# Kernel optimization log

Hardware: AMD Instinct MI355X
Metric: run time of the kernel (lower is better)

## Reference

```python
import jax, jax.numpy as jnp
import numpy as np

B, S, D_IN, D_CODE, K = 8, 4096, 1024, 64, 4096


def setup_inputs() -> dict:
    key = jax.random.key(0)
    k1, k2, k3, k4 = jax.random.split(key, 4)
    return {
        "input": jax.random.normal(k1, (B, S, D_IN), dtype=jnp.float32),
        "W_send": jax.random.normal(k2, (D_IN, D_CODE), dtype=jnp.float32) * (1.0 / np.sqrt(D_IN)),
        "b_send": jnp.zeros((D_CODE,), dtype=jnp.float32),
        "emb": jax.random.normal(k3, (K, D_CODE), dtype=jnp.float32),
        "W_recv": jax.random.normal(k4, (D_CODE, D_IN), dtype=jnp.float32) * (1.0 / np.sqrt(D_CODE)),
        "b_recv": jnp.zeros((D_IN,), dtype=jnp.float32),
    }


def reference(input, W_send, b_send, emb, W_recv, b_recv):
    # encoder: z = send(input) -> [B, S, D_CODE]
    z = jnp.einsum('bsi,ic->bsc', input, W_send) + b_send

    # VQEmbedding.lookup: argmin_k ||e_k||^2 - 2 <z, e_k>  (no-grad path)
    sqr = jnp.sum(emb * emb, axis=1)                      # [K]
    cov = jnp.einsum('bsc,kc->bsk', z, emb)               # [B, S, K]
    indices = jnp.argmin(sqr - 2.0 * cov, axis=-1)        # [B, S] int

    # fetch embeddings (gather)
    vectors = emb[indices]                                # [B, S, D_CODE]

    # straight-through estimator: values = z + sg(vectors - z)
    values = z + jax.lax.stop_gradient(vectors - z)

    # decoder: x = recv(values) -> [B, S, D_IN]
    x = jnp.einsum('bsc,ci->bsi', values, W_recv) + b_recv

    # VQEmbedding.loss (reduction='sum')
    embedding_loss = jnp.sum((vectors - jax.lax.stop_gradient(z)) ** 2)
    commitment_loss = jnp.sum((z - jax.lax.stop_gradient(vectors)) ** 2)

    # empirical code entropy in bits
    num_codes = emb.shape[0]
    counts = jnp.bincount(indices.ravel(), length=num_codes)
    p = counts.astype(jnp.float32) / jnp.float32(indices.size)
    ent = -jnp.sum(jnp.where(p > 0, p * jnp.log(jnp.where(p > 0, p, 1.0)), 0.0)) / jnp.log(2.0)

    return x, indices, embedding_loss, commitment_loss, ent
```

## Files before the change

### kernel.cpp

```cpp
#include <hip/hip_runtime.h>

#define DIN 1024
#define DC 64
#define KC 4096

typedef _Float16 f16x8 __attribute__((ext_vector_type(8)));
typedef _Float16 f16x4 __attribute__((ext_vector_type(4)));
typedef float f32x4 __attribute__((ext_vector_type(4)));

__device__ __forceinline__ void gll16(const void* g, void* l) {
    __builtin_amdgcn_global_load_lds(
        (const __attribute__((address_space(1))) unsigned int*)g,
        (__attribute__((address_space(3))) unsigned int*)l, 16, 0, 0);
}

__global__ __launch_bounds__(256) void k_prep(const float* __restrict__ emb,
                                              const float* __restrict__ Ws,
                                              const float* __restrict__ Wr,
                                              _Float16* __restrict__ Ee,
                                              float* __restrict__ sqr,
                                              _Float16* __restrict__ Wh,
                                              _Float16* __restrict__ WrT,
                                              int* __restrict__ counts) {
    int b = blockIdx.x;
    int tid = threadIdx.x;
    if (b < 1024) {
        int code = b * 4 + (tid >> 6);
        int lane = tid & 63;
        float v = emb[(size_t)code * DC + lane];
        Ee[(size_t)code * 64 + lane] = (_Float16)v;
        float s = v * v;
        #pragma unroll
        for (int m = 1; m < 64; m <<= 1) s += __shfl_xor(s, m);
        if (lane == 0) sqr[code] = s;
        if (tid < 4) counts[b * 4 + tid] = 0;
        return;
    }
    if (b < 1040) {
        int k0 = (b - 1024) * 64;
        #pragma unroll
        for (int it = 0; it < 16; ++it) {
            int q = it * 256 + tid;
            int c = q >> 6, kl = q & 63;
            float v = Ws[(size_t)(k0 + kl) * 64 + c];
            Wh[(size_t)c * 1024 + k0 + kl] = (_Float16)v;
        }
        return;
    }
    int b2 = b - 1040;
    #pragma unroll
    for (int it = 0; it < 16; ++it) {
        int k = it * 4 + (tid >> 6);
        int rr = b2 * 64 + (tid & 63);
        WrT[(size_t)rr * 64 + k] = (_Float16)Wr[(size_t)k * 1024 + rr];
    }
}

__global__ __launch_bounds__(256) void k_main(const float* __restrict__ in,
                                              const _Float16* __restrict__ Wh,
                                              const float* __restrict__ bs,
                                              const _Float16* __restrict__ Ee,
                                              const float* __restrict__ sqr,
                                              int* __restrict__ idx,
                                              float* __restrict__ out_idx,
                                              int* __restrict__ counts,
                                              float* __restrict__ lpart) {
    __shared__ char smem[32768];
    const int tid = threadIdx.x;
    const int row0 = blockIdx.x * 64;
    const int wid = tid >> 6, lane = tid & 63;
    const int c15 = lane & 15, g = lane >> 4;
    const int g16 = g * 16;
    const int wm = wid >> 1, wn = wid & 1;

    f32x4 acc[2][2];
    const f32x4 zz4 = {0.f, 0.f, 0.f, 0.f};
    #pragma unroll
    for (int mf = 0; mf < 2; ++mf)
        #pragma unroll
        for (int nf = 0; nf < 2; ++nf) acc[mf][nf] = zz4;

    int abyte[2], aswz[2], bbyte[2], bswz[2];
    #pragma unroll
    for (int mf = 0; mf < 2; ++mf) {
        int r = wm * 32 + mf * 16 + c15;
        abyte[mf] = r * 128; aswz[mf] = (r & 7) << 4;
    }
    #pragma unroll
    for (int nf = 0; nf < 2; ++nf) {
        int c = wn * 32 + nf * 16 + c15;
        bbyte[nf] = c * 128; bswz[nf] = (c & 7) << 4;
    }

    auto stageB = [&](int buf, int s) {
        char* dst = smem + buf * 16384 + 8192;
        #pragma unroll
        for (int r = 0; r < 2; ++r) {
            int p = r * 4096 + wid * 1024 + lane * 16;
            int row = p >> 7, off = p & 127;
            int soff = off ^ ((row & 7) << 4);
            gll16((const char*)Wh + (size_t)row * 2048 + s * 128 + soff,
                  dst + p);
        }
    };
    auto loadA = [&](int s, float4* a) {
        #pragma unroll
        for (int it = 0; it < 4; ++it) {
            int q = it * 256 + tid;
            int r = q >> 4, c4 = q & 15;
            a[it] = *(const float4*)&in[(size_t)(row0 + r) * DIN + s * 64 + c4 * 4];
        }
    };
    auto writeA = [&](int buf, const float4* a) {
        char* Ah = smem + buf * 16384;
        #pragma unroll
        for (int it = 0; it < 4; ++it) {
            int q = it * 256 + tid;
            int r = q >> 4, c4 = q & 15;
            float v[4] = {a[it].x, a[it].y, a[it].z, a[it].w};
            f16x4 h;
            #pragma unroll
            for (int j = 0; j < 4; ++j) h[j] = (_Float16)v[j];
            int o = r * 128 + ((c4 * 8) ^ ((r & 7) << 4));
            *(f16x4*)(Ah + o) = h;
        }
    };
    auto compute = [&](int buf) {
        const char* Ah = smem + buf * 16384;
        const char* Bh = Ah + 8192;
        #pragma unroll
        for (int ks = 0; ks < 2; ++ks) {
            int koff = ks * 64 + g16;
            f16x8 bh[2];
            #pragma unroll
            for (int nf = 0; nf < 2; ++nf)
                bh[nf] = *(const f16x8*)(Bh + bbyte[nf] + (koff ^ bswz[nf]));
            #pragma unroll
            for (int mf = 0; mf < 2; ++mf) {
                f16x8 ah = *(const f16x8*)(Ah + abyte[mf] + (koff ^ aswz[mf]));
                #pragma unroll
                for (int nf = 0; nf < 2; ++nf)
                    acc[mf][nf] = __builtin_amdgcn_mfma_f32_16x16x32_f16(
                        ah, bh[nf], acc[mf][nf], 0, 0, 0);
            }
        }
    };

    {
        float4 a0[4];
        loadA(0, a0);
        stageB(0, 0);
        writeA(0, a0);
    }
    __syncthreads();
    for (int s = 0; s < 16; ++s) {
        int c = s & 1;
        float4 an[4];
        if (s < 15) {
            loadA(s + 1, an);
            stageB(c ^ 1, s + 1);
        }
        compute(c);
        if (s < 15) writeA(c ^ 1, an);
        __syncthreads();
    }

    char* Zt = smem + 16384;
    #pragma unroll
    for (int nf = 0; nf < 2; ++nf) {
        int k = wn * 32 + nf * 16 + c15;
        float bias = bs[k];
        #pragma unroll
        for (int mf = 0; mf < 2; ++mf)
            #pragma unroll
            for (int r2 = 0; r2 < 4; ++r2) {
                int row = wm * 32 + mf * 16 + g * 4 + r2;
                _Float16 zh = (_Float16)(acc[mf][nf][r2] + bias);
                *(_Float16*)(Zt + row * 128 + ((k * 2) ^ ((row & 7) << 4))) = zh;
            }
    }
    __syncthreads();

    const int wm2 = wm, wn2 = wn;
    f16x8 zfh[2][2];
    #pragma unroll
    for (int nf = 0; nf < 2; ++nf) {
        int zr = wn2 * 32 + nf * 16 + c15;
        int sw = (zr & 7) << 4;
        #pragma unroll
        for (int j = 0; j < 2; ++j)
            zfh[j][nf] = *(const f16x8*)(Zt + zr * 128 + ((j * 64 + g16) ^ sw));
    }

    int rbase[2], rx[2];
    #pragma unroll
    for (int mf = 0; mf < 2; ++mf) {
        int r = wm2 * 32 + mf * 16 + c15;
        rbase[mf] = r * 128;
        rx[mf] = (r & 7) << 4;
    }

    auto stageE = [&](int ch, int buf) {
        char* dst = smem + buf * 8192;
        const char* src = (const char*)Ee + (size_t)ch * 8192;
        #pragma unroll
        for (int t = 0; t < 2; ++t) {
            int p = t * 4096 + tid * 16;
            int r = p >> 7, off = p & 127;
            gll16(src + r * 128 + (off ^ ((r & 7) << 4)), dst + p);
        }
    };

    float bv[2];
    int   bi[2];
    #pragma unroll
    for (int nf = 0; nf < 2; ++nf) { bv[nf] = 3.402823466e38f; bi[nf] = 0; }

    stageE(0, 0);
    __syncthreads();

    for (int ch = 0; ch < 64; ++ch) {
        const int buf = ch & 1;
        f32x4 sqv[2];
        #pragma unroll
        for (int mf = 0; mf < 2; ++mf)
            sqv[mf] = *(const f32x4*)(sqr + ch * 64 + wm2 * 32 + mf * 16 + g * 4);

        if (ch < 63) stageE(ch + 1, buf ^ 1);

        const char* base = smem + buf * 8192;
        f32x4 sacc[2][2];
        #pragma unroll
        for (int j = 0; j < 2; ++j) {
            const int kbyte = j * 64 + g16;
            f16x8 af[2];
            #pragma unroll
            for (int mf = 0; mf < 2; ++mf)
                af[mf] = *(const f16x8*)(base + rbase[mf] + (kbyte ^ rx[mf]));
            #pragma unroll
            for (int mf = 0; mf < 2; ++mf)
                #pragma unroll
                for (int nf = 0; nf < 2; ++nf)
                    sacc[mf][nf] = __builtin_amdgcn_mfma_f32_16x16x32_f16(
                        af[mf], zfh[j][nf],
                        j == 0 ? zz4 : sacc[mf][nf], 0, 0, 0);
        }

        #pragma unroll
        for (int nf = 0; nf < 2; ++nf) {
            #pragma unroll
            for (int mf = 0; mf < 2; ++mf) {
                f32x4 v = sqv[mf] - sacc[mf][nf] * 2.0f;
                #pragma unroll
                for (int r2 = 0; r2 < 4; ++r2) {
                    if (v[r2] < bv[nf]) {
                        bv[nf] = v[r2];
                        bi[nf] = ch * 64 + wm2 * 32 + mf * 16 + g * 4 + r2;
                    }
                }
            }
        }
        __syncthreads();
    }

    float* redv = (float*)(smem + 24576);
    int*   redi = (int*)(smem + 25088);
    float* zsqa = (float*)(smem + 25600);

    #pragma unroll
    for (int nf = 0; nf < 2; ++nf) {
        float v_ = bv[nf]; int i_ = bi[nf];
        #pragma unroll
        for (int m = 16; m <= 32; m <<= 1) {
            float ov = __shfl_xor(v_, m);
            int oi = __shfl_xor(i_, m);
            if (ov < v_ || (ov == v_ && oi < i_)) { v_ = ov; i_ = oi; }
        }
        if (g == 0) {
            int rl = wn2 * 32 + nf * 16 + c15;
            redv[wm2 * 64 + rl] = v_;
            redi[wm2 * 64 + rl] = i_;
        }
    }
    if (wm2 == 0) {
        #pragma unroll
        for (int nf = 0; nf < 2; ++nf) {
            float s = 0.f;
            #pragma unroll
            for (int j = 0; j < 2; ++j)
                #pragma unroll
                for (int e = 0; e < 8; ++e) {
                    float zv = (float)zfh[j][nf][e];
                    s += zv * zv;
                }
            s += __shfl_xor(s, 16);
            s += __shfl_xor(s, 32);
            if (g == 0) zsqa[wn2 * 32 + nf * 16 + c15] = s;
        }
    }
    __syncthreads();
    if (tid < 64) {
        float v0 = redv[tid]; int i0 = redi[tid];
        float v1 = redv[64 + tid]; int i1 = redi[64 + tid];
        if (v1 < v0 || (v1 == v0 && i1 < i0)) { v0 = v1; i0 = i1; }
        int grow = row0 + tid;
        idx[grow] = i0;
        out_idx[grow] = (float)i0;
        atomicAdd(&counts[i0], 1);
        float lossv = v0 + zsqa[tid];
        #pragma unroll
        for (int m = 1; m < 64; m <<= 1) lossv += __shfl_xor(lossv, m);
        if (tid == 0) lpart[blockIdx.x] = lossv;
    }
}

__global__ __launch_bounds__(256) void k_recv(const _Float16* __restrict__ Ee,
                                              const _Float16* __restrict__ WrT,
                                              const float* __restrict__ br,
                                              const int* __restrict__ idx,
                                              const int* __restrict__ counts,
                                              const float* __restrict__ lpart,
                                              float* __restrict__ x,
                                              float* __restrict__ out_sc) {
    __shared__ char smem[24832];
    int tid = threadIdx.x;

    if (blockIdx.x == 512) {
        float* red = (float*)smem;
        red[tid] = lpart[tid] + lpart[256 + tid];
        __syncthreads();
        for (int s = 128; s > 0; s >>= 1) {
            if (tid < s) red[tid] += red[tid + s];
            __syncthreads();
        }
        float loss = red[0];
        __syncthreads();
        float ep = 0.f;
        for (int k = tid; k < KC; k += 256) {
            int c = counts[k];
            if (c > 0) {
                float p = (float)c / 32768.0f;
                ep += p * logf(p);
            }
        }
        red[tid] = ep; __syncthreads();
        for (int s = 128; s > 0; s >>= 1) {
            if (tid < s) red[tid] += red[tid + s];
            __syncthreads();
        }
        if (tid == 0) {
            out_sc[0] = loss;
            out_sc[1] = loss;
            out_sc[2] = -red[0] * 1.4426950408889634f;
        }
        return;
    }

    const int row0 = blockIdx.x * 64;
    const int wid = tid >> 6, lane = tid & 63;
    const int c15 = lane & 15, g = lane >> 4;
    const int g16 = g * 16;
    int* sidx = (int*)(smem + 24576);

    if (tid < 64) sidx[tid] = idx[row0 + tid];
    __syncthreads();

    #pragma unroll
    for (int t = 0; t < 2; ++t) {
        int p = t * 4096 + tid * 16;
        int r = p >> 7, off = p & 127;
        gll16((const char*)Ee + (size_t)sidx[r] * 128 + (off ^ ((r & 7) << 4)),
              smem + p);
    }

    auto stageW = [&](int cc, int buf) {
        char* dst = smem + 8192 + buf * 8192;
        #pragma unroll
        for (int t = 0; t < 2; ++t) {
            int p = t * 4096 + tid * 16;
            int r = p >> 7, off = p & 127;
            gll16((const char*)WrT + (size_t)(cc * 64 + r) * 128
                      + (off ^ ((r & 7) << 4)),
                  dst + p);
        }
    };
    stageW(0, 0);
    __syncthreads();

    int abase[4], ax[4];
    #pragma unroll
    for (int mf = 0; mf < 4; ++mf) {
        int r = mf * 16 + c15;
        abase[mf] = r * 128;
        ax[mf] = (r & 7) << 4;
    }
    const int brow = wid * 16 + c15;
    const int bbase = 8192 + brow * 128;
    const int bx = (brow & 7) << 4;

    const f32x4 zz4 = {0.f, 0.f, 0.f, 0.f};
    for (int cc = 0; cc < 16; ++cc) {
        const int buf = cc & 1;
        if (cc < 15) stageW(cc + 1, buf ^ 1);

        const int col = cc * 64 + wid * 16 + c15;
        float bias = br[col];

        f32x4 acc[4];
        #pragma unroll
        for (int j = 0; j < 2; ++j) {
            const int kbyte = j * 64 + g16;
            f16x8 bf = *(const f16x8*)(smem + buf * 8192 + bbase + (kbyte ^ bx));
            #pragma unroll
            for (int mf = 0; mf < 4; ++mf) {
                f16x8 af = *(const f16x8*)(smem + abase[mf] + (kbyte ^ ax[mf]));
                acc[mf] = __builtin_amdgcn_mfma_f32_16x16x32_f16(
                    af, bf, j == 0 ? zz4 : acc[mf], 0, 0, 0);
            }
        }

        #pragma unroll
        for (int mf = 0; mf < 4; ++mf)
            #pragma unroll
            for (int r2 = 0; r2 < 4; ++r2)
                x[(size_t)(row0 + mf * 16 + g * 4 + r2) * DIN + col]
                    = acc[mf][r2] + bias;

        __syncthreads();
    }
}

extern "C" void kernel_launch(void* const* d_in, const int* in_sizes, int n_in,
                              void* d_out, int out_size, void* d_ws, size_t ws_size,
                              hipStream_t stream) {
    (void)in_sizes; (void)n_in; (void)out_size; (void)ws_size;
    const float* input  = (const float*)d_in[0];
    const float* W_send = (const float*)d_in[1];
    const float* b_send = (const float*)d_in[2];
    const float* emb    = (const float*)d_in[3];
    const float* W_recv = (const float*)d_in[4];
    const float* b_recv = (const float*)d_in[5];
    float* out = (float*)d_out;

    char* ws = (char*)d_ws;
    _Float16* Ee  = (_Float16*)(ws);
    float*    sqr = (float*)(ws + 524288);
    int*      idx = (int*)  (ws + 540672);
    int*   counts = (int*)  (ws + 671744);
    float* lpart  = (float*)(ws + 688128);
    _Float16* Wh  = (_Float16*)(ws + 690176);
    _Float16* WrT = (_Float16*)(ws + 821248);

    float* out_x   = out;
    float* out_idx = out + 33554432;
    float* out_sc  = out + 33587200;

    k_prep<<<1056, 256, 0, stream>>>(emb, W_send, W_recv, Ee, sqr, Wh, WrT, counts);
    k_main<<<512, 256, 0, stream>>>(input, Wh, b_send, Ee, sqr,
                                    idx, out_idx, counts, lpart);
    k_recv<<<513, 256, 0, stream>>>(Ee, WrT, b_recv, idx, counts, lpart,
                                    out_x, out_sc);
}
```

Baseline: 91.01 us.

## Load codebook fragments directly into registers instead of staging through LDS

The codebook scan now has each lane read its MFMA operand fragments and squared norms straight from global memory. The next chunk is prefetched into registers while the current one is being computed. This removes the LDS double buffer and the per-chunk block barrier. In exchange, waves sharing the same row half load duplicate data, and the scan now depends on L2 latency and bandwidth rather than LDS.

```diff
diff --git a/kernel.cpp b/kernel.cpp
--- a/kernel.cpp
+++ b/kernel.cpp
@@ -72,9 +72,9 @@
     const int c15 = lane & 15, g = lane >> 4;
     const int g16 = g * 16;
     const int wm = wid >> 1, wn = wid & 1;
+    const f32x4 zz4 = {0.f, 0.f, 0.f, 0.f};
 
     f32x4 acc[2][2];
-    const f32x4 zz4 = {0.f, 0.f, 0.f, 0.f};
     #pragma unroll
     for (int mf = 0; mf < 2; ++mf)
         #pragma unroll
@@ -125,7 +125,7 @@
             *(f16x4*)(Ah + o) = h;
         }
     };
-    auto compute = [&](int buf) {
+    auto computeS = [&](int buf) {
         const char* Ah = smem + buf * 16384;
         const char* Bh = Ah + 8192;
         #pragma unroll
@@ -160,7 +160,7 @@
             loadA(s + 1, an);
             stageB(c ^ 1, s + 1);
         }
-        compute(c);
+        computeS(c);
         if (s < 15) writeA(c ^ 1, an);
         __syncthreads();
     }
@@ -175,76 +175,64 @@
             #pragma unroll
             for (int r2 = 0; r2 < 4; ++r2) {
                 int row = wm * 32 + mf * 16 + g * 4 + r2;
-                _Float16 zh = (_Float16)(acc[mf][nf][r2] + bias);
-                *(_Float16*)(Zt + row * 128 + ((k * 2) ^ ((row & 7) << 4))) = zh;
+                *(_Float16*)(Zt + row * 128 + ((k * 2) ^ ((row & 7) << 4)))
+                    = (_Float16)(acc[mf][nf][r2] + bias);
             }
     }
     __syncthreads();
 
-    const int wm2 = wm, wn2 = wn;
     f16x8 zfh[2][2];
     #pragma unroll
     for (int nf = 0; nf < 2; ++nf) {
-        int zr = wn2 * 32 + nf * 16 + c15;
+        int zr = wn * 32 + nf * 16 + c15;
         int sw = (zr & 7) << 4;
         #pragma unroll
         for (int j = 0; j < 2; ++j)
             zfh[j][nf] = *(const f16x8*)(Zt + zr * 128 + ((j * 64 + g16) ^ sw));
     }
 
-    int rbase[2], rx[2];
-    #pragma unroll
-    for (int mf = 0; mf < 2; ++mf) {
-        int r = wm2 * 32 + mf * 16 + c15;
-        rbase[mf] = r * 128;
-        rx[mf] = (r & 7) << 4;
-    }
-
-    auto stageE = [&](int ch, int buf) {
-        char* dst = smem + buf * 8192;
-        const char* src = (const char*)Ee + (size_t)ch * 8192;
-        #pragma unroll
-        for (int t = 0; t < 2; ++t) {
-            int p = t * 4096 + tid * 16;
-            int r = p >> 7, off = p & 127;
-            gll16(src + r * 128 + (off ^ ((r & 7) << 4)), dst + p);
-        }
-    };
+    const _Float16* ebase = Ee + ((size_t)(wm * 32 + c15)) * 64 + g * 8;
 
     float bv[2];
     int   bi[2];
     #pragma unroll
     for (int nf = 0; nf < 2; ++nf) { bv[nf] = 3.402823466e38f; bi[nf] = 0; }
 
-    stageE(0, 0);
-    __syncthreads();
+    f16x8 af[2][2];
+    f32x4 sqv[2];
+    #pragma unroll
+    for (int mf = 0; mf < 2; ++mf) {
+        #pragma unroll
+        for (int j = 0; j < 2; ++j)
+            af[mf][j] = *(const f16x8*)(ebase + mf * 1024 + j * 32);
+        sqv[mf] = *(const f32x4*)(sqr + wm * 32 + mf * 16 + g * 4);
+    }
 
     for (int ch = 0; ch < 64; ++ch) {
-        const int buf = ch & 1;
-        f32x4 sqv[2];
-        #pragma unroll
-        for (int mf = 0; mf < 2; ++mf)
-            sqv[mf] = *(const f32x4*)(sqr + ch * 64 + wm2 * 32 + mf * 16 + g * 4);
-
-        if (ch < 63) stageE(ch + 1, buf ^ 1);
-
-        const char* base = smem + buf * 8192;
+        f16x8 an2[2][2];
+        f32x4 sqn[2];
+        if (ch < 63) {
+            const _Float16* eb = ebase + (size_t)(ch + 1) * 4096;
+            #pragma unroll
+            for (int mf = 0; mf < 2; ++mf) {
+                #pragma unroll
+                for (int j = 0; j < 2; ++j)
+                    an2[mf][j] = *(const f16x8*)(eb + mf * 1024 + j * 32);
+                sqn[mf] = *(const f32x4*)(sqr + (ch + 1) * 64 + wm * 32
+                                          + mf * 16 + g * 4);
+            }
+        }
+
         f32x4 sacc[2][2];
         #pragma unroll
-        for (int j = 0; j < 2; ++j) {
-            const int kbyte = j * 64 + g16;
-            f16x8 af[2];
-            #pragma unroll
-            for (int mf = 0; mf < 2; ++mf)
-                af[mf] = *(const f16x8*)(base + rbase[mf] + (kbyte ^ rx[mf]));
+        for (int j = 0; j < 2; ++j)
             #pragma unroll
             for (int mf = 0; mf < 2; ++mf)
                 #pragma unroll
                 for (int nf = 0; nf < 2; ++nf)
                     sacc[mf][nf] = __builtin_amdgcn_mfma_f32_16x16x32_f16(
-                        af[mf], zfh[j][nf],
+                        af[mf][j], zfh[j][nf],
                         j == 0 ? zz4 : sacc[mf][nf], 0, 0, 0);
-        }
 
         #pragma unroll
         for (int nf = 0; nf < 2; ++nf) {
@@ -255,12 +243,21 @@
                 for (int r2 = 0; r2 < 4; ++r2) {
                     if (v[r2] < bv[nf]) {
                         bv[nf] = v[r2];
-                        bi[nf] = ch * 64 + wm2 * 32 + mf * 16 + g * 4 + r2;
+                        bi[nf] = ch * 64 + wm * 32 + mf * 16 + g * 4 + r2;
                     }
                 }
             }
         }
-        __syncthreads();
+
+        if (ch < 63) {
+            #pragma unroll
+            for (int mf = 0; mf < 2; ++mf) {
+                #pragma unroll
+                for (int j = 0; j < 2; ++j)
+                    af[mf][j] = an2[mf][j];
+                sqv[mf] = sqn[mf];
+            }
+        }
     }
 
     float* redv = (float*)(smem + 24576);
@@ -277,12 +274,12 @@
             if (ov < v_ || (ov == v_ && oi < i_)) { v_ = ov; i_ = oi; }
         }
         if (g == 0) {
-            int rl = wn2 * 32 + nf * 16 + c15;
-            redv[wm2 * 64 + rl] = v_;
-            redi[wm2 * 64 + rl] = i_;
-        }
-    }
-    if (wm2 == 0) {
+            int rl = wn * 32 + nf * 16 + c15;
+            redv[wm * 64 + rl] = v_;
+            redi[wm * 64 + rl] = i_;
+        }
+    }
+    if (wm == 0) {
         #pragma unroll
         for (int nf = 0; nf < 2; ++nf) {
             float s = 0.f;
@@ -295,7 +292,7 @@
                 }
             s += __shfl_xor(s, 16);
             s += __shfl_xor(s, 32);
-            if (g == 0) zsqa[wn2 * 32 + nf * 16 + c15] = s;
+            if (g == 0) zsqa[wn * 32 + nf * 16 + c15] = s;
         }
     }
     __syncthreads();
```

Result: slower. 116.8 us (+28.4%).
